# Optimization experiments

Hardware: AMD Instinct MI355X
Metric: run time of the kernel (lower is better)

## Reference

```python
import jax, jax.numpy as jnp
import numpy as np

# RGA_Module(in_channel=128, in_spatial=784, use_spatial=True, use_channel=True,
#            cha_ratio=4, spa_ratio=4, down_ratio=4), BatchNorm in eval mode with
# running_mean=0, running_var=1 folded into per-channel scale/shift (s, b).
B, C, H, W = 64, 128, 28, 28
S = H * W            # 784
IC = C // 4          # 32  inter_channel
IS = S // 4          # 196 inter_spatial
DS = (1 + IS) // 4   # 49  W_spatial bottleneck
DC = (1 + IC) // 4   # 8   W_channel bottleneck


def setup_inputs() -> dict:
    key = jax.random.key(0)
    ks = iter(jax.random.split(key, 40))
    def wgt(shape):
        return jax.random.normal(next(ks), shape, jnp.float32) * 0.05
    def scale(c):
        return 1.0 + 0.1 * jax.random.normal(next(ks), (c,), jnp.float32)
    def shift(c):
        return 0.1 * jax.random.normal(next(ks), (c,), jnp.float32)

    inp = {"x": jax.random.normal(next(ks), (B, C, H, W), jnp.float32)}
    for name, shape in [("th_w", (IC, C)), ("ph_w", (IC, C)), ("ggs_w", (IS, 2 * S)),
                        ("gxs_w", (IC, C)), ("ws1_w", (DS, 1 + IS)), ("ws2_w", (1, DS)),
                        ("thc_w", (IS, S)), ("phc_w", (IS, S)), ("ggc_w", (IC, 2 * C)),
                        ("gxc_w", (IS, S)), ("wc1_w", (DC, 1 + IC)), ("wc2_w", (1, DC))]:
        inp[name] = wgt(shape)
    for name, ch in [("th", IC), ("ph", IC), ("ggs", IS), ("gxs", IC), ("ws1", DS),
                     ("ws2", 1), ("thc", IS), ("phc", IS), ("ggc", IC), ("gxc", IS),
                     ("wc1", DC), ("wc2", 1)]:
        inp[name + "_s"] = scale(ch)
        inp[name + "_b"] = shift(ch)
    return inp


def _bn(y, s, b):
    # eval-mode BatchNorm2d with running stats folded: per-channel affine
    return y * s[None, :, None, None] + b[None, :, None, None]


def _cbr(y, Wc, s, b):
    # 1x1 Conv (no bias) + BN(eval) + ReLU
    return jax.nn.relu(_bn(jnp.einsum('oc,bchw->bohw', Wc, y), s, b))


def reference(x, th_w, th_s, th_b, ph_w, ph_s, ph_b, ggs_w, ggs_s, ggs_b,
              gxs_w, gxs_s, gxs_b, ws1_w, ws1_s, ws1_b, ws2_w, ws2_s, ws2_b,
              thc_w, thc_s, thc_b, phc_w, phc_s, phc_b, ggc_w, ggc_s, ggc_b,
              gxc_w, gxc_s, gxc_b, wc1_w, wc1_s, wc1_b, wc2_w, wc2_s, wc2_b):
    b, c, h, w = x.shape
    hw = h * w
    # ---- spatial relation-aware attention ----
    theta = _cbr(x, th_w, th_s, th_b).reshape(b, -1, hw)   # [b, IC, hw]
    phi = _cbr(x, ph_w, ph_s, ph_b).reshape(b, -1, hw)     # [b, IC, hw]
    Gs = jnp.einsum('bci,bcj->bij', theta, phi)            # [b, hw, hw]
    Gs_in = jnp.transpose(Gs, (0, 2, 1)).reshape(b, hw, h, w)
    Gs_out = Gs.reshape(b, hw, h, w)
    Gs_joint = _cbr(jnp.concatenate([Gs_in, Gs_out], 1), ggs_w, ggs_s, ggs_b)  # [b, IS, h, w]
    g_xs = jnp.mean(_cbr(x, gxs_w, gxs_s, gxs_b), axis=1, keepdims=True)       # [b, 1, h, w]
    ys = jnp.concatenate([g_xs, Gs_joint], 1)                                  # [b, 1+IS, h, w]
    W_ys = _bn(jnp.einsum('oc,bchw->bohw', ws2_w, _cbr(ys, ws1_w, ws1_s, ws1_b)),
               ws2_s, ws2_b)                                                   # [b, 1, h, w]
    x = jax.nn.sigmoid(W_ys) * x
    # ---- channel relation-aware attention ----
    xc = jnp.transpose(x.reshape(b, c, hw), (0, 2, 1))[..., None]              # [b, hw, c, 1]
    theta_c = jnp.transpose(_cbr(xc, thc_w, thc_s, thc_b)[..., 0], (0, 2, 1))  # [b, c, IS]
    phi_c = _cbr(xc, phc_w, phc_s, phc_b)[..., 0]                              # [b, IS, c]
    Gc = jnp.einsum('bcs,bsd->bcd', theta_c, phi_c)                            # [b, c, c]
    Gc_joint = _cbr(jnp.concatenate([jnp.transpose(Gc, (0, 2, 1))[..., None],
                                     Gc[..., None]], 1), ggc_w, ggc_s, ggc_b)  # [b, IC, c, 1]
    g_xc = jnp.mean(_cbr(xc, gxc_w, gxc_s, gxc_b), axis=1, keepdims=True)      # [b, 1, c, 1]
    yc = jnp.concatenate([g_xc, Gc_joint], 1)                                  # [b, 1+IC, c, 1]
    W_yc = _bn(jnp.einsum('oc,bchw->bohw', wc2_w, _cbr(yc, wc1_w, wc1_s, wc1_b)),
               wc2_s, wc2_b)                                                   # [b, 1, c, 1]
    W_yc = jnp.transpose(W_yc, (0, 2, 1, 3))                                   # [b, c, 1, 1]
    return jax.nn.sigmoid(W_yc) * x
```

## Files before the change

### kernel.cpp

```cpp
#include <hip/hip_runtime.h>
#include <hip/hip_bf16.h>
#include <math.h>


#define BB 64
#define CC 128
#define HW 784
#define IC 32
#define IS 196
#define DS 49

#define O_THW 0
#define O_PHW 4096
#define O_GGSW 8192
#define O_GXSW 315520
#define O_WS1W 319616
#define O_WS2W 329272
#define O_THCW 329324
#define O_PHCW 482988
#define O_GGCW 636652
#define O_GXCW 644844
#define O_WC1W 798508
#define O_WC2W 798772
#define O_THS 798780
#define O_THB 798812
#define O_PHS 798844
#define O_PHB 798876
#define O_GGSS 798908
#define O_GGSB 799104
#define O_GXSS 799300
#define O_GXSB 799332
#define O_WS1S 799364
#define O_WS1B 799416
#define O_WS2S 799468
#define O_WS2B 799472
#define O_THCS 799476
#define O_THCB 799672
#define O_PHCS 799868
#define O_PHCB 800064
#define O_GGCS 800260
#define O_GGCB 800292
#define O_GXCS 800324
#define O_GXCB 800520
#define O_WC1S 800716
#define O_WC1B 800724
#define O_WC2S 800732
#define O_WC2B 800736
#define WF_TOTAL 800768

static const int SRC_SIZES[36] = {
  4096,4096,307328,4096,9653,49,153664,153664,8192,153664,264,8,
  32,32,32,32,196,196,32,32,49,49,1,1,196,196,196,196,32,32,196,196,8,8,1,1};
static const int DST_OFF[36] = {
  O_THW,O_PHW,O_GGSW,O_GXSW,O_WS1W,O_WS2W,O_THCW,O_PHCW,O_GGCW,O_GXCW,O_WC1W,O_WC2W,
  O_THS,O_THB,O_PHS,O_PHB,O_GGSS,O_GGSB,O_GXSS,O_GXSB,O_WS1S,O_WS1B,O_WS2S,O_WS2B,
  O_THCS,O_THCB,O_PHCS,O_PHCB,O_GGCS,O_GGCB,O_GXCS,O_GXCB,O_WC1S,O_WC1B,O_WC2S,O_WC2B};

struct ConvArgs { const void* p[36]; int cum[37]; int dst[36]; };

typedef __attribute__((ext_vector_type(8))) short short8;
typedef __attribute__((ext_vector_type(4))) float fragf4;

union FragU { unsigned int w[4]; short8 s8; };

__device__ __forceinline__ float sigf(float v){ return 1.0f/(1.0f+expf(-v)); }
__device__ __forceinline__ float hb2f(unsigned short h){ return __uint_as_float(((unsigned)h)<<16); }
__device__ __forceinline__ unsigned short f2hb(float v){
  __hip_bfloat16 hb = __float2bfloat16(v);
  return *reinterpret_cast<unsigned short*>(&hb);
}
__device__ __forceinline__ float loadx(const void* x, int flag, size_t idx){
  if (flag) return hb2f(((const unsigned short*)x)[idx]);
  return ((const float*)x)[idx];
}

__global__ void kd_detect(const void* x, int* flag){
  __shared__ int cnt[256];
  int t = threadIdx.x;
  const unsigned short* h = (const unsigned short*)x;
  int c = 0;
  for (int k=0;k<4;k++){
    unsigned short v = h[t*4+k];
    int e = (v>>7)&0xFF;
    c += (e==0 || (e>=97 && e<=157)) ? 1 : 0;
  }
  cnt[t] = c;
  __syncthreads();
  for (int s=128; s; s>>=1){ if (t<s) cnt[t]+=cnt[t+s]; __syncthreads(); }
  if (t==0) *flag = (cnt[0] >= 973) ? 1 : 0;
}

__global__ void kc_convert(ConvArgs a, const int* flagp, float* wf){
  int flag = *flagp;
  int g = blockIdx.x*256 + threadIdx.x;
  if (g >= a.cum[36]) return;
  int i = 0;
  while (g >= a.cum[i+1]) i++;
  int local = g - a.cum[i];
  float v;
  if (flag) v = hb2f(((const unsigned short*)a.p[i])[local]);
  else      v = ((const float*)a.p[i])[local];
  wf[a.dst[i] + local] = v;
}

#define KW_TOT (5*IS*HW + 96*CC)
__global__ void kw_wbf(const float* wf, unsigned short* wbf){
  int i = blockIdx.x*256 + threadIdx.x;
  if (i >= KW_TOT) return;
  float v;
  if (i < 3*IS*HW){
    int which = i/(IS*HW), r = i - which*(IS*HW);
    int off = which==0?O_THCW:(which==1?O_PHCW:O_GXCW);
    v = wf[off + r];
  } else if (i < 5*IS*HW){
    int which = i/(IS*HW), r = i - which*(IS*HW);
    int row = r/HW, col = r - row*HW;
    v = wf[O_GGSW + row*(2*HW) + (which-3)*HW + col];
  } else {
    int r = i - 5*IS*HW;
    int row = r >> 7, col = r & 127;
    v = (row < 64) ? wf[row*CC + col] : wf[O_GXSW + (row-64)*CC + col];
  }
  wbf[i] = f2hb(v);
}

__global__ void k0_ws1bf(const float* wf, unsigned int* ws1bf32){
  int i = blockIdx.x*256 + threadIdx.x;
  if (i >= 64*112) return;
  int o2 = i/112, k2 = i - o2*112;
  int k = k2*2;
  float v0 = (o2<DS && k<197)   ? wf[O_WS1W + o2*197 + k]   : 0.f;
  float v1 = (o2<DS && k+1<197) ? wf[O_WS1W + o2*197 + k+1] : 0.f;
  ws1bf32[i] = (unsigned)f2hb(v0) | ((unsigned)f2hb(v1)<<16);
}

#define XST 68
__global__ __launch_bounds__(256) void k1k2_mfma(const void* x, const int* flagp,
    const float* wf, const unsigned short* wthph, unsigned short* thph, float* g_xs)
{
  __shared__ __align__(16) unsigned int Xl[64*XST];
  int flag = *flagp;
  int t = threadIdx.x;
  int pt = blockIdx.x % 13, b = blockIdx.x / 13;
  int p0 = pt*64;

  #pragma unroll
  for (int k=0; k<8; k++){
    int idx = k*256 + t;
    int q = idx & 31;
    int c2 = idx >> 5;
    int p = p0 + 2*q, c = 2*c2;
    unsigned int w0 = 0u, w1 = 0u;
    if (p < HW){
      if (flag){
        const unsigned short* xb = (const unsigned short*)x + (size_t)b*CC*HW;
        unsigned int a0 = *(const unsigned int*)(xb + (size_t)c*HW + p);
        unsigned int a1 = *(const unsigned int*)(xb + (size_t)(c+1)*HW + p);
        w0 = (a0 & 0xffffu) | (a1 << 16);
        w1 = (a0 >> 16) | (a1 & 0xffff0000u);
      } else {
        const float* xb = (const float*)x + (size_t)b*CC*HW;
        float2 a0 = *(const float2*)(xb + (size_t)c*HW + p);
        float2 a1 = *(const float2*)(xb + (size_t)(c+1)*HW + p);
        w0 = (unsigned)f2hb(a0.x) | ((unsigned)f2hb(a1.x)<<16);
        w1 = (unsigned)f2hb(a0.y) | ((unsigned)f2hb(a1.y)<<16);
      }
    }
    Xl[(2*q+0)*XST + c2] = w0;
    Xl[(2*q+1)*XST + c2] = w1;
  }
  __syncthreads();

  int lane = t & 63, w = t >> 6;
  int m16 = lane & 15, kq = lane >> 4;
  fragf4 acc[6];
  #pragma unroll
  for (int mt=0; mt<6; mt++)
    #pragma unroll
    for (int r=0;r<4;r++) acc[mt][r] = 0.f;

  const unsigned short* Xu = (const unsigned short*)Xl;
  #pragma unroll
  for (int kk=0; kk<4; kk++){
    short8 bfr = *(const short8*)(Xu + (w*16+m16)*(2*XST) + kk*32 + kq*8);
    #pragma unroll
    for (int mt=0; mt<6; mt++){
      short8 af = *(const short8*)(wthph + (mt*16+m16)*CC + kk*32 + kq*8);
      acc[mt] = __builtin_amdgcn_mfma_f32_16x16x32_bf16(af, bfr, acc[mt], 0,0,0);
    }
  }

  int p = p0 + w*16 + m16;
  #pragma unroll
  for (int mt=0; mt<4; mt++){
    #pragma unroll
    for (int r=0;r<4;r++){
      int o = mt*16 + kq*4 + r;
      float sc = (o<32) ? wf[O_THS+o] : wf[O_PHS+o-32];
      float sh = (o<32) ? wf[O_THB+o] : wf[O_PHB+o-32];
      float v = fmaxf(sc*acc[mt][r] + sh, 0.f);
      if (p < HW) thph[((size_t)b*64 + o)*HW + p] = f2hb(v);
    }
  }
  float gs = 0.f;
  #pragma unroll
  for (int mt=4; mt<6; mt++){
    #pragma unroll
    for (int r=0;r<4;r++){
      int o = (mt-4)*16 + kq*4 + r;
      gs += fmaxf(wf[O_GXSS+o]*acc[mt][r] + wf[O_GXSB+o], 0.f);
    }
  }
  gs += __shfl_xor(gs, 16);
  gs += __shfl_xor(gs, 32);
  if (kq == 0 && p < HW) g_xs[(size_t)b*HW + p] = gs*(1.f/32.f);
}

#define K3ST 40
__global__ __launch_bounds__(256) void k3_mfma(const unsigned short* wggs,
    const unsigned short* thph, unsigned short* acomb)
{
  __shared__ __align__(16) unsigned short Al[112*K3ST];
  __shared__ __align__(16) unsigned short Bl[32*K3ST];
  int t = threadIdx.x;
  int mh = blockIdx.x & 1;
  int b  = (blockIdx.x >> 1) & 63;
  int which = blockIdx.x >> 7;
  int m0 = mh*112;
  const unsigned short* wsrc = wggs + (size_t)which*IS*HW;
  const unsigned short* ssrc = thph + ((size_t)b*64 + (which ? 0 : 32))*HW;
  int lane = t & 63, w = t >> 6;
  int m16 = lane & 15, kq = lane >> 4;
  fragf4 acc[2][2];
  #pragma unroll
  for (int i=0;i<2;i++)
    #pragma unroll
    for (int nt=0;nt<2;nt++)
      #pragma unroll
      for (int r=0;r<4;r++) acc[i][nt][r] = 0.f;

  for (int kk=0; kk<25; kk++){
    int p0 = kk*32;
    __syncthreads();
    for (int i=t; i<112*4; i+=256){
      int row = i>>2, q = i&3;
      uint4 v = make_uint4(0u,0u,0u,0u);
      int gr = m0 + row, p = p0 + q*8;
      if (gr < IS && p+8 <= HW)
        v = *(const uint4*)(wsrc + (size_t)gr*HW + p);
      *(uint4*)(Al + row*K3ST + q*8) = v;
    }
    if (t < 128){
      int row = t>>2, q = t&3;
      uint4 v = make_uint4(0u,0u,0u,0u);
      int p = p0 + q*8;
      if (p+8 <= HW)
        v = *(const uint4*)(ssrc + (size_t)row*HW + p);
      *(uint4*)(Bl + row*K3ST + q*8) = v;
    }
    __syncthreads();
    short8 bfr[2];
    #pragma unroll
    for (int nt=0;nt<2;nt++)
      bfr[nt] = *(const short8*)(Bl + (nt*16+m16)*K3ST + kq*8);
    #pragma unroll
    for (int i=0;i<2;i++){
      int mt = w + 4*i;
      if (mt < 7){
        short8 af = *(const short8*)(Al + (mt*16+m16)*K3ST + kq*8);
        acc[i][0] = __builtin_amdgcn_mfma_f32_16x16x32_bf16(af, bfr[0], acc[i][0], 0,0,0);
        acc[i][1] = __builtin_amdgcn_mfma_f32_16x16x32_bf16(af, bfr[1], acc[i][1], 0,0,0);
      }
    }
  }
  unsigned short* dst = acomb + (size_t)b*208*64 + which*32;
  #pragma unroll
  for (int i=0;i<2;i++){
    int mt = w + 4*i;
    if (mt >= 7) continue;
    #pragma unroll
    for (int r=0;r<4;r++){
      int o = m0 + mt*16 + kq*4 + r;
      if (o >= IS) continue;
      #pragma unroll
      for (int nt=0;nt<2;nt++){
        int c = nt*16 + m16;
        dst[(size_t)o*64 + c] = f2hb(acc[i][nt][r]);
      }
    }
  }
}

#define A4ST 72
#define ALS 33
#define GTS 113
union K4Sh {
  struct { unsigned short Al16[208*A4ST]; unsigned int Sl[64*ALS]; } s1;
  unsigned int Gt[64*GTS];
};
__global__ __launch_bounds__(256,3) void k4_mfma(const void* x, const int* flagp,
    const float* wf, const unsigned short* thph,
    const unsigned short* acomb, const float* g_xs,
    const unsigned int* ws1bf32, unsigned short* x1tp)
{
  __shared__ K4Sh sh;
  __shared__ float ash[64];
  int flag = *flagp;
  int t = threadIdx.x;
  int pt = blockIdx.x % 13, b = blockIdx.x / 13;
  int p0 = pt*64;
  int lane = t & 63, w = t >> 6;
  int col = lane & 15, kq = lane >> 4;

  const unsigned short* Ab16 = acomb + (size_t)b*208*64;
  for (int i=t; i<208*8; i+=256){
    int row = i>>3, q = i&7;
    uint4 v = make_uint4(0u,0u,0u,0u);
    if (row < IS) v = *(const uint4*)(Ab16 + (size_t)row*64 + q*8);
    *(uint4*)(sh.s1.Al16 + (size_t)row*A4ST + q*8) = v;
  }
  const unsigned short* tb = thph + (size_t)b*64*HW;
  for (int i=t; i<32*32; i+=256){
    int c2 = i>>5, q = i&31;
    int p = p0 + 2*q;
    unsigned int w0 = 0u, w1 = 0u;
    if (p < HW){
      int c = 2*c2;
      unsigned int a0 = *(const unsigned int*)(tb + (size_t)c*HW + p);
      unsigned int a1 = *(const unsigned int*)(tb + (size_t)(c+1)*HW + p);
      w0 = (a0 & 0xffffu) | (a1 << 16);
      w1 = (a0 >> 16) | (a1 & 0xffff0000u);
    }
    sh.s1.Sl[(2*q+0)*ALS + c2] = w0;
    sh.s1.Sl[(2*q+1)*ALS + c2] = w1;
  }
  __syncthreads();

  fragf4 acc1[13];
  #pragma unroll
  for (int nt=0; nt<13; nt++)
    #pragma unroll
    for (int r=0;r<4;r++) acc1[nt][r] = 0.f;
  #pragma unroll
  for (int kk=0; kk<2; kk++){
    FragU af;
    #pragma unroll
    for (int q=0;q<4;q++) af.w[q] = sh.s1.Sl[(w*16+col)*ALS + kk*16 + kq*4 + q];
    #pragma unroll
    for (int nt=0; nt<13; nt++){
      short8 bf8 = *(const short8*)(sh.s1.Al16 + (size_t)(nt*16+col)*A4ST + kk*32 + kq*8);
      acc1[nt] = __builtin_amdgcn_mfma_f32_16x16x32_bf16(af.s8, bf8, acc1[nt], 0,0,0);
    }
  }
  __syncthreads();

  unsigned short* Gt16 = (unsigned short*)sh.Gt;
  for (int i=t; i<64*9; i+=256){
    int pp = i/9, q = i - pp*9;
    sh.Gt[pp*GTS + 104 + q] = 0u;
  }
  if (t < 64){
    int p = p0 + t;
    float gx = (p < HW) ? g_xs[b*HW + p] : 0.f;
    Gt16[t*226 + 0] = f2hb(gx);
  }
  #pragma unroll
  for (int nt=0; nt<13; nt++){
    int o = nt*16 + col;
    float sc = wf[O_GGSS + o], shf = wf[O_GGSB + o];
    #pragma unroll
    for (int r=0;r<4;r++){
      int pp = w*16 + kq*4 + r;
      float g = fmaxf(sc*acc1[nt][r] + shf, 0.f);
      Gt16[pp*226 + 1 + o] = f2hb(g);
    }
  }
  __syncthreads();

  fragf4 acc2[4];
  #pragma unroll
  for (int nt=0; nt<4; nt++)
    #pragma unroll
    for (int r=0;r<4;r++) acc2[nt][r] = 0.f;
  #pragma unroll
  for (int kk=0; kk<7; kk++){
    FragU af;
    #pragma unroll
    for (int q=0;q<4;q++) af.w[q] = sh.Gt[(w*16+col)*GTS + kk*16 + kq*4 + q];
    #pragma unroll
    for (int nt=0; nt<4; nt++){
      FragU bf;
      #pragma unroll
      for (int q=0;q<4;q++) bf.w[q] = ws1bf32[(nt*16+col)*112 + kk*16 + kq*4 + q];
      acc2[nt] = __builtin_amdgcn_mfma_f32_16x16x32_bf16(af.s8, bf.s8, acc2[nt], 0,0,0);
    }
  }

  float wys[4] = {0.f,0.f,0.f,0.f};
  #pragma unroll
  for (int nt=0; nt<4; nt++){
    int o2 = nt*16 + col;
    bool vd = (o2 < DS);
    float s1 = vd ? wf[O_WS1S+o2] : 0.f;
    float b1 = vd ? wf[O_WS1B+o2] : 0.f;
    float w2 = vd ? wf[O_WS2W+o2] : 0.f;
    #pragma unroll
    for (int r=0;r<4;r++){
      float z = fmaxf(s1*acc2[nt][r] + b1, 0.f);
      wys[r] += w2*z;
    }
  }
  #pragma unroll
  for (int m=1; m<16; m<<=1){
    #pragma unroll
    for (int r=0;r<4;r++) wys[r] += __shfl_xor(wys[r], m, 16);
  }
  if (col == 0){
    float s2 = wf[O_WS2S], b2 = wf[O_WS2B];
    #pragma unroll
    for (int r=0;r<4;r++){
      int pp = w*16 + kq*4 + r;
      ash[pp] = sigf(s2*wys[r] + b2);
    }
  }
  __syncthreads();

  for (int i=t; i<CC*16; i+=256){
    int c = i>>4, q = i&15;
    int p = p0 + q*4;
    if (p < HW){
      float a0 = ash[q*4+0], a1 = ash[q*4+1], a2 = ash[q*4+2], a3 = ash[q*4+3];
      size_t base = (size_t)b*CC*HW + (size_t)c*HW + p;
      float v0,v1,v2,v3;
      if (flag){
        uint2 u = *(const uint2*)((const unsigned short*)x + base);
        v0 = a0*hb2f((unsigned short)(u.x & 0xffff));
        v1 = a1*hb2f((unsigned short)(u.x >> 16));
        v2 = a2*hb2f((unsigned short)(u.y & 0xffff));
        v3 = a3*hb2f((unsigned short)(u.y >> 16));
      } else {
        float4 xv = *(const float4*)((const float*)x + base);
        v0 = a0*xv.x; v1 = a1*xv.y; v2 = a2*xv.z; v3 = a3*xv.w;
      }
      uint2 o2;
      o2.x = (unsigned)f2hb(v0) | ((unsigned)f2hb(v1)<<16);
      o2.y = (unsigned)f2hb(v2) | ((unsigned)f2hb(v3)<<16);
      *(uint2*)(x1tp + base) = o2;
    }
  }
}

#define KST 40
__global__ __launch_bounds__(256) void k8_mfma(const unsigned short* wbf,
    const unsigned short* x1tp, const float* wf, float* outp)
{
  __shared__ __align__(16) unsigned short Al[48*KST];
  __shared__ __align__(16) unsigned short Bl[128*KST];
  int t = threadIdx.x;
  int j = blockIdx.x & 63;
  int b = (j&7)*8 + (j>>3);
  int mt = blockIdx.x >> 6;
  int m0 = mt*48;
  const unsigned short* xsrc = x1tp + (size_t)b*CC*HW;
  int lane = t & 63, w = t >> 6;
  int m16 = lane & 15, kq = lane >> 4;
  fragf4 acc[3][2];
  #pragma unroll
  for (int st=0; st<3; st++)
    #pragma unroll
    for (int ct=0; ct<2; ct++)
      #pragma unroll
      for (int r=0; r<4; r++) acc[st][ct][r] = 0.f;

  for (int kk=0; kk<25; kk++){
    int p0 = kk*32;
    __syncthreads();
    if (t < 192){
      int row = t>>2, q = t&3;
      uint4 v = make_uint4(0u,0u,0u,0u);
      int g = m0 + row, p = p0 + q*8;
      if (g < 3*IS && p+8 <= HW)
        v = *(const uint4*)(wbf + (size_t)g*HW + p);
      *(uint4*)(Al + row*KST + q*8) = v;
    }
    for (int i=t; i<128*4; i+=256){
      int row = i>>2, q = i&3;
      uint4 v = make_uint4(0u,0u,0u,0u);
      int p = p0 + q*8;
      if (p+8 <= HW)
        v = *(const uint4*)(xsrc + (size_t)row*HW + p);
      *(uint4*)(Bl + row*KST + q*8) = v;
    }
    __syncthreads();
    short8 bfr[2];
    #pragma unroll
    for (int ct=0; ct<2; ct++){
      int n = (w*2+ct)*16 + m16;
      bfr[ct] = *(const short8*)(Bl + n*KST + kq*8);
    }
    #pragma unroll
    for (int st=0; st<3; st++){
      short8 af = *(const short8*)(Al + (st*16+m16)*KST + kq*8);
      acc[st][0] = __builtin_amdgcn_mfma_f32_16x16x32_bf16(af, bfr[0], acc[st][0], 0,0,0);
      acc[st][1] = __builtin_amdgcn_mfma_f32_16x16x32_bf16(af, bfr[1], acc[st][1], 0,0,0);
    }
  }
  #pragma unroll
  for (int st=0; st<3; st++){
    #pragma unroll
    for (int r=0; r<4; r++){
      int g = m0 + st*16 + kq*4 + r;
      if (g >= 3*IS) continue;
      int which = (g >= 2*IS) ? 2 : (g >= IS ? 1 : 0);
      int s = g - which*IS;
      int so = (which==2) ? O_GXCS : O_THCS + which*392;
      float sc = wf[so + s], sh = wf[so + 196 + s];
      float* dst = outp + (size_t)which*(64*IS*CC) + ((size_t)b*IS + s)*CC;
      #pragma unroll
      for (int ct=0; ct<2; ct++){
        int c = (w*2+ct)*16 + m16;
        dst[c] = fmaxf(sc*acc[st][ct][r] + sh, 0.f);
      }
    }
  }
}

__global__ __launch_bounds__(256) void k9_bfact(const float* wf, const float* thcp,
    const float* phcp, float* Bph, float* Bth)
{
  __shared__ __align__(16) float wtl[32*32*4];
  int t = threadIdx.x;
  int sq = blockIdx.x & 3;
  int b  = (blockIdx.x >> 2) & 63;
  int which = blockIdx.x >> 8;
  for (int i = t; i < 32*32; i += 256){
    int jc = i >> 5, o = i & 31;
    *(float4*)(wtl + i*4) =
        *(const float4*)(wf + O_GGCW + o*256 + which*CC + jc*4);
  }
  __syncthreads();
  const float* src = which ? thcp : phcp;
  float* dst = which ? Bth : Bph;
  int o = t & 31, sloc = t >> 5;
  int s0 = sq*49;
  float acc[7];
  #pragma unroll
  for (int k=0;k<7;k++) acc[k]=0.f;
  const float* srow[7];
  #pragma unroll
  for (int k=0;k<7;k++){
    int sl = sloc + 8*k;
    srow[k] = src + ((size_t)b*IS + s0 + (sl<49 ? sl : 0))*CC;
  }
  for (int jc=0; jc<32; jc++){
    float4 wv = *(const float4*)(wtl + (jc*32+o)*4);
    #pragma unroll
    for (int k=0;k<7;k++){
      if (sloc + 8*k < 49){
        float4 sv = *(const float4*)(srow[k] + jc*4);
        acc[k] += wv.x*sv.x + wv.y*sv.y + wv.z*sv.z + wv.w*sv.w;
      }
    }
  }
  #pragma unroll
  for (int k=0;k<7;k++){
    int sl = sloc + 8*k;
    if (sl < 49){
      dst[((size_t)b*IS + s0 + sl)*IC + o] = acc[k];
    }
  }
}

__global__ __launch_bounds__(256) void k10a_part(const float* thcp, const float* phcp,
    const float* gxcp, const float* Bph, const float* Bth,
    float* part, float* gxp)
{
  int t = threadIdx.x;
  int d = t & 127, oh = t >> 7;
  int sc = blockIdx.x % 14, b = blockIdx.x / 14;
  int s0 = sc*14;
  float acc[16];
  #pragma unroll
  for (int o=0;o<16;o++) acc[o]=0.f;
  float gxa = 0.f;
  for (int i=0;i<14;i++){
    int s = s0 + i;
    size_t base = ((size_t)b*IS + s)*CC + d;
    float tv = thcp[base], pv = phcp[base];
    if (oh == 0) gxa += gxcp[base];
    const float* bp = Bph + ((size_t)b*IS + s)*IC + oh*16;
    const float* bt = Bth + ((size_t)b*IS + s)*IC + oh*16;
    #pragma unroll
    for (int o=0;o<16;o++) acc[o] += bp[o]*tv + bt[o]*pv;
  }
  float* pb = part + (((size_t)b*14 + sc)*IC + oh*16)*CC + d;
  #pragma unroll
  for (int o=0;o<16;o++) pb[(size_t)o*CC] = acc[o];
  if (oh == 0) gxp[((size_t)b*14 + sc)*CC + d] = gxa;
}

__global__ void k10b_catt(const float* wf, const float* part, const float* gxp,
                          float* c_att)
{
  int idx = blockIdx.x*256 + threadIdx.x;
  int d = idx & 127;
  int b = idx >> 7;
  float acc[IC];
  #pragma unroll
  for (int o=0;o<IC;o++) acc[o]=0.f;
  float gx = 0.f;
  for (int sc=0; sc<14; sc++){
    gx += gxp[((size_t)b*14 + sc)*CC + d];
    const float* pb = part + ((size_t)b*14 + sc)*IC*CC + d;
    #pragma unroll
    for (int o=0;o<IC;o++) acc[o] += pb[(size_t)o*CC];
  }
  gx *= (1.f/196.f);
  #pragma unroll
  for (int o=0;o<IC;o++) acc[o] = fmaxf(wf[O_GGCS+o]*acc[o]+wf[O_GGCB+o], 0.f);
  float acc2 = 0.f;
  #pragma unroll
  for (int o2=0;o2<8;o2++){
    float tt = wf[O_WC1W + o2*33]*gx;
    #pragma unroll
    for (int o=0;o<IC;o++) tt += wf[O_WC1W + o2*33+1+o]*acc[o];
    float z = fmaxf(wf[O_WC1S+o2]*tt + wf[O_WC1B+o2], 0.f);
    acc2 += wf[O_WC2W+o2]*z;
  }
  c_att[idx] = sigf(wf[O_WC2S]*acc2 + wf[O_WC2B]);
}

__global__ void k12_final(const int* flagp, const unsigned int* x1tp2,
                          const float* c_att, void* out)
{
  int i = blockIdx.x*256 + threadIdx.x;
  int flag = *flagp;
  unsigned int v = x1tp2[i];
  float a = c_att[i/392];
  float v0 = a*hb2f((unsigned short)(v & 0xffff));
  float v1 = a*hb2f((unsigned short)(v >> 16));
  if (flag){
    ((unsigned int*)out)[i] = (unsigned)f2hb(v0) | ((unsigned)f2hb(v1)<<16);
  } else {
    ((float*)out)[2*i+0] = v0;
    ((float*)out)[2*i+1] = v1;
  }
}

extern "C" void kernel_launch(void* const* d_in, const int* in_sizes, int n_in,
                              void* d_out, int out_size, void* d_ws, size_t ws_size,
                              hipStream_t stream)
{
  const void* x = d_in[0];

  float* W = (float*)d_ws;
  int*   flag  = (int*)W;
  float* wf    = W + 64;
  float* theta = wf + WF_TOTAL;
  unsigned short* thph = (unsigned short*)(theta + 1605632);
  float* g_xs  = theta + 2*1605632;
  float* Aphi  = g_xs + 50176;
  float* Atheta= Aphi + 401408;
  unsigned short* acomb = (unsigned short*)Aphi;
  unsigned short* x1tp = (unsigned short*)(Atheta + 401408);
  float* thcp  = Atheta + 401408 + 3211264;
  float* phcp  = thcp + 1605632;
  float* gxcp  = phcp + 1605632;
  float* Bph   = gxcp + 1605632;
  float* Bth   = Bph + 401408;
  unsigned int* ws1bf32 = (unsigned int*)(Bth + 401408);
  float* c_att = (float*)(ws1bf32) + 9664;
  unsigned short* wbf = (unsigned short*)(c_att + 8192);
  unsigned short* wggs = wbf + 3*IS*HW;
  unsigned short* wthph = wbf + 5*IS*HW;
  float* part = theta;
  float* gxp  = theta + 3670016;

  ConvArgs ca;
  ca.cum[0] = 0;
  for (int i=0;i<36;i++){
    ca.p[i] = d_in[i+1];
    ca.cum[i+1] = ca.cum[i] + SRC_SIZES[i];
    ca.dst[i] = DST_OFF[i];
  }

  kd_detect<<<1, 256, 0, stream>>>(x, flag);
  kc_convert<<<(800716+255)/256, 256, 0, stream>>>(ca, flag, wf);
  kw_wbf<<<(KW_TOT+255)/256, 256, 0, stream>>>(wf, wbf);
  k0_ws1bf<<<(64*112+255)/256, 256, 0, stream>>>(wf, ws1bf32);
  k1k2_mfma<<<64*13, 256, 0, stream>>>(x, flag, wf, wthph, thph, g_xs);
  k3_mfma<<<2*64*2, 256, 0, stream>>>(wggs, thph, acomb);
  k4_mfma<<<64*13, 256, 0, stream>>>(x, flag, wf, thph, acomb,
      g_xs, ws1bf32, x1tp);
  k8_mfma<<<13*64, 256, 0, stream>>>(wbf, x1tp, wf, thcp);
  k9_bfact<<<2*64*4, 256, 0, stream>>>(wf, thcp, phcp, Bph, Bth);
  k10a_part<<<64*14, 256, 0, stream>>>(thcp, phcp, gxcp, Bph, Bth, part, gxp);
  k10b_catt<<<(BB*CC)/256, 256, 0, stream>>>(wf, part, gxp, c_att);
  k12_final<<<(BB*CC*HW/2)/256, 256, 0, stream>>>(flag, (const unsigned int*)x1tp,
      c_att, d_out);
}
```

Baseline: 332.8 us.

## Load MFMA operands directly from global memory, dropping LDS staging in k4 and k8

In k4_mfma the acomb B-operand is no longer staged into shared memory. Each lane reads its short8 fragment straight from global memory, which shrinks the LDS union and raises launch bounds occupancy from 3 to 4 blocks. In k8_mfma the per-iteration shared-memory tiles and both __syncthreads are removed, and A/B fragments are loaded directly from global memory with a bounds predicate. The earlier kernel now zero-fills rows 196..207 of acomb so the unguarded reads see zeros, and the kernels rely on L1/L2 to supply operand reuse that LDS used to provide.

```diff
diff --git a/kernel.cpp b/kernel.cpp
--- a/kernel.cpp
+++ b/kernel.cpp
@@ -73,6 +73,9 @@
   if (flag) return hb2f(((const unsigned short*)x)[idx]);
   return ((const float*)x)[idx];
 }
+__device__ __forceinline__ short8 zero8(){
+  FragU z; z.w[0]=0u; z.w[1]=0u; z.w[2]=0u; z.w[3]=0u; return z.s8;
+}
 
 __global__ void kd_detect(const void* x, int* flag){
   __shared__ int cnt[256];
@@ -281,24 +284,23 @@
     #pragma unroll
     for (int r=0;r<4;r++){
       int o = m0 + mt*16 + kq*4 + r;
-      if (o >= IS) continue;
+      if (o >= 208) continue;
       #pragma unroll
       for (int nt=0;nt<2;nt++){
         int c = nt*16 + m16;
-        dst[(size_t)o*64 + c] = f2hb(acc[i][nt][r]);
+        dst[(size_t)o*64 + c] = (o < IS) ? f2hb(acc[i][nt][r]) : (unsigned short)0;
       }
     }
   }
 }
 
-#define A4ST 72
 #define ALS 33
 #define GTS 113
 union K4Sh {
-  struct { unsigned short Al16[208*A4ST]; unsigned int Sl[64*ALS]; } s1;
+  unsigned int Sl[64*ALS];
   unsigned int Gt[64*GTS];
 };
-__global__ __launch_bounds__(256,3) void k4_mfma(const void* x, const int* flagp,
+__global__ __launch_bounds__(256,4) void k4_mfma(const void* x, const int* flagp,
     const float* wf, const unsigned short* thph,
     const unsigned short* acomb, const float* g_xs,
     const unsigned int* ws1bf32, unsigned short* x1tp)
@@ -312,13 +314,6 @@
   int lane = t & 63, w = t >> 6;
   int col = lane & 15, kq = lane >> 4;
 
-  const unsigned short* Ab16 = acomb + (size_t)b*208*64;
-  for (int i=t; i<208*8; i+=256){
-    int row = i>>3, q = i&7;
-    uint4 v = make_uint4(0u,0u,0u,0u);
-    if (row < IS) v = *(const uint4*)(Ab16 + (size_t)row*64 + q*8);
-    *(uint4*)(sh.s1.Al16 + (size_t)row*A4ST + q*8) = v;
-  }
   const unsigned short* tb = thph + (size_t)b*64*HW;
   for (int i=t; i<32*32; i+=256){
     int c2 = i>>5, q = i&31;
@@ -331,11 +326,12 @@
       w0 = (a0 & 0xffffu) | (a1 << 16);
       w1 = (a0 >> 16) | (a1 & 0xffff0000u);
     }
-    sh.s1.Sl[(2*q+0)*ALS + c2] = w0;
-    sh.s1.Sl[(2*q+1)*ALS + c2] = w1;
+    sh.Sl[(2*q+0)*ALS + c2] = w0;
+    sh.Sl[(2*q+1)*ALS + c2] = w1;
   }
   __syncthreads();
 
+  const unsigned short* Ab16 = acomb + (size_t)b*208*64 + (size_t)col*64 + kq*8;
   fragf4 acc1[13];
   #pragma unroll
   for (int nt=0; nt<13; nt++)
@@ -345,10 +341,10 @@
   for (int kk=0; kk<2; kk++){
     FragU af;
     #pragma unroll
-    for (int q=0;q<4;q++) af.w[q] = sh.s1.Sl[(w*16+col)*ALS + kk*16 + kq*4 + q];
+    for (int q=0;q<4;q++) af.w[q] = sh.Sl[(w*16+col)*ALS + kk*16 + kq*4 + q];
     #pragma unroll
     for (int nt=0; nt<13; nt++){
-      short8 bf8 = *(const short8*)(sh.s1.Al16 + (size_t)(nt*16+col)*A4ST + kk*32 + kq*8);
+      short8 bf8 = *(const short8*)(Ab16 + (size_t)nt*16*64 + kk*32);
       acc1[nt] = __builtin_amdgcn_mfma_f32_16x16x32_bf16(af.s8, bf8, acc1[nt], 0,0,0);
     }
   }
@@ -450,20 +446,19 @@
   }
 }
 
-#define KST 40
 __global__ __launch_bounds__(256) void k8_mfma(const unsigned short* wbf,
     const unsigned short* x1tp, const float* wf, float* outp)
 {
-  __shared__ __align__(16) unsigned short Al[48*KST];
-  __shared__ __align__(16) unsigned short Bl[128*KST];
   int t = threadIdx.x;
   int j = blockIdx.x & 63;
   int b = (j&7)*8 + (j>>3);
   int mt = blockIdx.x >> 6;
   int m0 = mt*48;
-  const unsigned short* xsrc = x1tp + (size_t)b*CC*HW;
   int lane = t & 63, w = t >> 6;
   int m16 = lane & 15, kq = lane >> 4;
+  const unsigned short* arow = wbf + (size_t)(m0 + m16)*HW + kq*8;
+  const unsigned short* brow = x1tp + (size_t)b*CC*HW + (size_t)(w*32 + m16)*HW + kq*8;
+  short8 zz = zero8();
   fragf4 acc[3][2];
   #pragma unroll
   for (int st=0; st<3; st++)
@@ -473,36 +468,19 @@
       for (int r=0; r<4; r++) acc[st][ct][r] = 0.f;
 
   for (int kk=0; kk<25; kk++){
-    int p0 = kk*32;
-    __syncthreads();
-    if (t < 192){
-      int row = t>>2, q = t&3;
-      uint4 v = make_uint4(0u,0u,0u,0u);
-      int g = m0 + row, p = p0 + q*8;
-      if (g < 3*IS && p+8 <= HW)
-        v = *(const uint4*)(wbf + (size_t)g*HW + p);
-      *(uint4*)(Al + row*KST + q*8) = v;
-    }
-    for (int i=t; i<128*4; i+=256){
-      int row = i>>2, q = i&3;
-      uint4 v = make_uint4(0u,0u,0u,0u);
-      int p = p0 + q*8;
-      if (p+8 <= HW)
-        v = *(const uint4*)(xsrc + (size_t)row*HW + p);
-      *(uint4*)(Bl + row*KST + q*8) = v;
-    }
-    __syncthreads();
-    short8 bfr[2];
-    #pragma unroll
-    for (int ct=0; ct<2; ct++){
-      int n = (w*2+ct)*16 + m16;
-      bfr[ct] = *(const short8*)(Bl + n*KST + kq*8);
-    }
+    int p = kk*32 + kq*8;
+    bool ok = (p + 8 <= HW);
+    short8 af[3], bfr[2];
+    #pragma unroll
+    for (int st=0; st<3; st++)
+      af[st] = ok ? *(const short8*)(arow + (size_t)st*16*HW + kk*32) : zz;
+    #pragma unroll
+    for (int ct=0; ct<2; ct++)
+      bfr[ct] = ok ? *(const short8*)(brow + (size_t)ct*16*HW + kk*32) : zz;
     #pragma unroll
     for (int st=0; st<3; st++){
-      short8 af = *(const short8*)(Al + (st*16+m16)*KST + kq*8);
-      acc[st][0] = __builtin_amdgcn_mfma_f32_16x16x32_bf16(af, bfr[0], acc[st][0], 0,0,0);
-      acc[st][1] = __builtin_amdgcn_mfma_f32_16x16x32_bf16(af, bfr[1], acc[st][1], 0,0,0);
+      acc[st][0] = __builtin_amdgcn_mfma_f32_16x16x32_bf16(af[st], bfr[0], acc[st][0], 0,0,0);
+      acc[st][1] = __builtin_amdgcn_mfma_f32_16x16x32_bf16(af[st], bfr[1], acc[st][1], 0,0,0);
     }
   }
   #pragma unroll
```

Measured after the change: 340.6 us. +2.4%, slower.
